# Kernel optimization log

Measured on AMD Instinct MI355X. Metric: run time of the kernel, lower is better.

Reference implementation:

```python
import jax, jax.numpy as jnp
import numpy as np

B = 8192
I = 1024
H = 1024


def setup_inputs() -> dict:
    key = jax.random.key(0)
    ks = jax.random.split(key, 7)
    s_in = 1.0 / np.sqrt(I)
    s_h = 1.0 / np.sqrt(H)
    return {
        "x_current": jax.random.normal(ks[0], (B, I), dtype=jnp.float32),
        "c_previous": jax.random.normal(ks[1], (B, H), dtype=jnp.float32),
        "h_previous": jax.random.normal(ks[2], (B, H), dtype=jnp.float32),
        # stacked gate weights, order (i, f, o, g); equivalent to 8 small nn.Linear
        "Wx": jax.random.normal(ks[3], (4 * H, I), dtype=jnp.float32) * s_in,
        "bx": jax.random.normal(ks[4], (4 * H,), dtype=jnp.float32) * s_in,
        "Wh": jax.random.normal(ks[5], (4 * H, H), dtype=jnp.float32) * s_h,
        "bh": jax.random.normal(ks[6], (4 * H,), dtype=jnp.float32) * s_h,
    }


def reference(x_current, c_previous, h_previous, Wx, bx, Wh, bh):
    # two fused GEMMs covering all 8 original linears: [B, 4H]
    gates = (jnp.einsum("bi,gi->bg", x_current, Wx) + bx
             + jnp.einsum("bh,gh->bg", h_previous, Wh) + bh)
    i_g, f_g, o_g, g_g = jnp.split(gates, 4, axis=-1)
    input_gate = jax.nn.sigmoid(i_g)
    forget_gate = jax.nn.sigmoid(f_g)
    output_gate = jax.nn.sigmoid(o_g)
    g_current = jnp.tanh(g_g)
    c_current = forget_gate * c_previous + input_gate * g_current
    h_current = output_gate * jnp.tanh(c_current)
    return (c_current, h_current)
```

## Files before the change

### kernel.cpp

```cpp
#include <hip/hip_runtime.h>
#include <hip/hip_bf16.h>

#define Bsz 8192
#define Isz 1024
#define Hsz 1024
#define Ksz 2048
#define Nsz 4096

#define BM 256
#define BN 256
#define BK 64
#define NT (Ksz / BK)

typedef __attribute__((ext_vector_type(8))) short bf16x8;
typedef __attribute__((ext_vector_type(4))) float f32x4;
typedef __attribute__((ext_vector_type(8))) unsigned short ushort8;

__device__ __forceinline__ void async_copy16(const void* g, void* l) {
  __builtin_amdgcn_global_load_lds(
      (const __attribute__((address_space(1))) void*)g,
      (__attribute__((address_space(3))) void*)l, 16, 0, 0);
}

__device__ __forceinline__ float fast_rcp(float x) {
  return __builtin_amdgcn_rcpf(x);
}
__device__ __forceinline__ float sigmoid_f(float x) {
  return fast_rcp(1.0f + __expf(-x));
}
__device__ __forceinline__ float tanh_f(float x) {
  x = fminf(15.0f, fmaxf(-15.0f, x));
  const float e = __expf(-2.0f * x);
  return (1.0f - e) * fast_rcp(1.0f + e);
}

__device__ __forceinline__ unsigned short bfc(float f) {
  return __builtin_bit_cast(unsigned short, __float2bfloat16(f));
}
__device__ __forceinline__ ushort8 cvt8v(float4 v0, float4 v1) {
  ushort8 o;
  o[0] = bfc(v0.x); o[1] = bfc(v0.y); o[2] = bfc(v0.z); o[3] = bfc(v0.w);
  o[4] = bfc(v1.x); o[5] = bfc(v1.y); o[6] = bfc(v1.z); o[7] = bfc(v1.w);
  return o;
}

__global__ __launch_bounds__(256) void prep_kernel(
    const float* __restrict__ x, const float* __restrict__ h,
    const float* __restrict__ Wx, const float* __restrict__ Wh,
    const float* __restrict__ bx, const float* __restrict__ bh,
    __hip_bfloat16* __restrict__ Abf, __hip_bfloat16* __restrict__ Wbf,
    float* __restrict__ bsum) {
  const int idx = blockIdx.x * 256 + threadIdx.x;
  const int ATH = (Bsz * Ksz) / 8;
  if (idx < ATH) {
    const int b = idx >> 8;
    const int k = (idx & 255) << 3;
    const float* src = (k < Isz) ? (x + (size_t)b * Isz + k)
                                 : (h + (size_t)b * Hsz + (k - Isz));
    const float4 v0 = ((const float4*)src)[0];
    const float4 v1 = ((const float4*)src)[1];
    *(ushort8*)(Abf + (size_t)b * Ksz + k) = cvt8v(v0, v1);
  } else {
    const int t2 = idx - ATH;
    const int r = t2 >> 8;
    const int k = (t2 & 255) << 3;
    const int hh = r >> 2, g = r & 3;
    const float* src = (k < Isz) ? (Wx + (size_t)(g * Hsz + hh) * Isz + k)
                                 : (Wh + (size_t)(g * Hsz + hh) * Hsz + (k - Isz));
    const float4 v0 = ((const float4*)src)[0];
    const float4 v1 = ((const float4*)src)[1];
    *(ushort8*)(Wbf + (size_t)r * Ksz + k) = cvt8v(v0, v1);
  }
  if (idx < Nsz) {
    const int hh = idx >> 2, g = idx & 3;
    bsum[idx] = bx[g * Hsz + hh] + bh[g * Hsz + hh];
  }
}

__global__ __launch_bounds__(512, 2) void lstm_gemm_kernel(
    const __hip_bfloat16* __restrict__ A,
    const __hip_bfloat16* __restrict__ W,
    const float* __restrict__ bsum,
    const float* __restrict__ c_prev,
    float* __restrict__ c_out,
    float* __restrict__ h_out) {
  __shared__ ulong2 smem_raw[8192];
  __hip_bfloat16* const As = (__hip_bfloat16*)smem_raw;
  __hip_bfloat16* const Bs = As + 2 * BM * BK;
  char* const smemc = (char*)smem_raw;

  const int tid = threadIdx.x;
  const int lane = tid & 63;
  const int wave = tid >> 6;
  const int wm = wave >> 2;
  const int wn = wave & 3;

  const int orig = blockIdx.x;
  const int swz = (orig & 7) * 64 + (orig >> 3);
  const int bx = swz & 31;
  const int by = swz >> 5;
  const int row0 = bx * BM;
  const int col0 = by * BN;

  const __hip_bfloat16* const Ag = A + (size_t)row0 * Ksz;
  const __hip_bfloat16* const Wg = W + (size_t)col0 * Ksz;

  const int sr = tid >> 3;
  const int so = ((tid & 7) ^ (sr & 7)) << 3;

  auto stage = [&](const __hip_bfloat16* gsrc, char* lhalf) {
#pragma unroll
    for (int p = 0; p < 2; ++p)
      async_copy16(gsrc + (size_t)(sr + p * 64) * Ksz,
                   lhalf + (tid + p * 512) * 16);
  };

  const int q = lane >> 4;
  const int cl = lane & 15;
  const int phi = cl & 7;
  const int swz0 = ((0 + q) ^ phi) << 3;
  const int swz1 = ((4 + q) ^ phi) << 3;
  const int aoff0 = (wm * 128 + cl) * BK + swz0;
  const int aoff1 = (wm * 128 + cl) * BK + swz1;
  const int boff0 = (wn * 64 + cl) * BK + swz0;
  const int boff1 = (wn * 64 + cl) * BK + swz1;

  stage(Ag + so, smemc);
  stage(Ag + (size_t)128 * Ksz + so, smemc + 16384);
  stage(Wg + so, smemc + 65536);
  stage(Wg + (size_t)128 * Ksz + so, smemc + 65536 + 16384);
  __builtin_amdgcn_sched_barrier(0);
  stage(Wg + BK + so, smemc + 65536 + 32768);
  stage(Wg + BK + (size_t)128 * Ksz + so, smemc + 65536 + 32768 + 16384);
  __builtin_amdgcn_sched_barrier(0);
  asm volatile("s_waitcnt vmcnt(4)" ::: "memory");
  __builtin_amdgcn_s_barrier();
  __builtin_amdgcn_sched_barrier(0);

  f32x4 acc[8][4] = {};

#define LDA(dst, m)                                                        \
  dst[0][0] = *(const bf16x8*)(Asb + aoff0 + (m) * (16 * BK));             \
  dst[0][1] = *(const bf16x8*)(Asb + aoff1 + (m) * (16 * BK));             \
  dst[1][0] = *(const bf16x8*)(Asb + aoff0 + ((m) + 1) * (16 * BK));       \
  dst[1][1] = *(const bf16x8*)(Asb + aoff1 + ((m) + 1) * (16 * BK));

#define CLUSTER(mi, p)                                                     \
  __builtin_amdgcn_s_setprio(1);                                           \
  _Pragma("unroll")                                                        \
  for (int n = 0; n < 4; ++n) {                                            \
    acc[mi][n] = __builtin_amdgcn_mfma_f32_16x16x32_bf16(                  \
        p[0][0], b0[n][0], acc[mi][n], 0, 0, 0);                           \
    acc[mi][n] = __builtin_amdgcn_mfma_f32_16x16x32_bf16(                  \
        p[0][1], b0[n][1], acc[mi][n], 0, 0, 0);                           \
    acc[(mi) + 1][n] = __builtin_amdgcn_mfma_f32_16x16x32_bf16(            \
        p[1][0], b0[n][0], acc[(mi) + 1][n], 0, 0, 0);                     \
    acc[(mi) + 1][n] = __builtin_amdgcn_mfma_f32_16x16x32_bf16(            \
        p[1][1], b0[n][1], acc[(mi) + 1][n], 0, 0, 0);                     \
  }                                                                        \
  __builtin_amdgcn_s_setprio(0);

  for (int t = 0; t < NT; ++t) {
    const __hip_bfloat16* const Asb = As + (t & 1) * (BM * BK);
    const __hip_bfloat16* const Bsb = Bs + (t & 1) * (BM * BK);
    char* const nA = smemc + (((t + 1) & 1) * 32768);
    char* const nB = smemc + 65536 + ((t & 1) * 32768);
    const int kA = (t + 1) * BK;
    const int kB = (t + 2) * BK;
    const bool doA = (t + 1) < NT;
    const bool doB = (t + 2) < NT;

    bf16x8 b0[4][2];
    bf16x8 aE[2][2], aO[2][2];

#pragma unroll
    for (int n = 0; n < 4; ++n) {
      b0[n][0] = *(const bf16x8*)(Bsb + boff0 + n * (16 * BK));
      b0[n][1] = *(const bf16x8*)(Bsb + boff1 + n * (16 * BK));
    }
    LDA(aE, 0)

    LDA(aO, 2)
    if (doA) stage(Ag + kA + so, nA);
    __builtin_amdgcn_sched_barrier(0);
    CLUSTER(0, aE)

    LDA(aE, 4)
    if (doA) stage(Ag + kA + (size_t)128 * Ksz + so, nA + 16384);
    __builtin_amdgcn_sched_barrier(0);
    CLUSTER(2, aO)

    __builtin_amdgcn_s_barrier();
    __builtin_amdgcn_sched_barrier(0);

    LDA(aO, 6)
    if (doB) stage(Wg + kB + so, nB);
    __builtin_amdgcn_sched_barrier(0);
    CLUSTER(4, aE)

    if (doB) stage(Wg + kB + (size_t)128 * Ksz + so, nB + 16384);
    __builtin_amdgcn_sched_barrier(0);
    CLUSTER(6, aO)

    if (t < NT - 2) {
      asm volatile("s_waitcnt vmcnt(4)" ::: "memory");
    } else if (t == NT - 2) {
      asm volatile("s_waitcnt vmcnt(0)" ::: "memory");
    }
    __builtin_amdgcn_s_barrier();
    __builtin_amdgcn_sched_barrier(0);
  }
#undef LDA
#undef CLUSTER

  __syncthreads();
  float* const E = (float*)smem_raw + wave * (16 * 68);

  float bj[4];
#pragma unroll
  for (int n = 0; n < 4; ++n)
    bj[n] = bsum[col0 + wn * 64 + n * 16 + cl];

  const int hw = (col0 >> 2) + wn * 16;
  const int r16 = lane >> 2;
  const int tt = lane & 3;

#pragma unroll
  for (int i = 0; i < 8; ++i) {
#pragma unroll
    for (int n = 0; n < 4; ++n)
#pragma unroll
      for (int r = 0; r < 4; ++r)
        E[(q * 4 + r) * 68 + n * 16 + cl] = acc[i][n][r] + bj[n];
    __builtin_amdgcn_wave_barrier();
    const float* Er = E + r16 * 68 + tt * 16;
    const float4 f0 = ((const float4*)Er)[0];
    const float4 f1 = ((const float4*)Er)[1];
    const float4 f2 = ((const float4*)Er)[2];
    const float4 f3 = ((const float4*)Er)[3];

    const int row = row0 + wm * 128 + i * 16 + r16;
    const size_t off = (size_t)row * Hsz + hw + tt * 4;
    const float4 cp4 = *(const float4*)(c_prev + off);
    float4 c4, h4;
    {
      const float cn = sigmoid_f(f0.y) * cp4.x + sigmoid_f(f0.x) * tanh_f(f0.w);
      c4.x = cn; h4.x = sigmoid_f(f0.z) * tanh_f(cn);
    }
    {
      const float cn = sigmoid_f(f1.y) * cp4.y + sigmoid_f(f1.x) * tanh_f(f1.w);
      c4.y = cn; h4.y = sigmoid_f(f1.z) * tanh_f(cn);
    }
    {
      const float cn = sigmoid_f(f2.y) * cp4.z + sigmoid_f(f2.x) * tanh_f(f2.w);
      c4.z = cn; h4.z = sigmoid_f(f2.z) * tanh_f(cn);
    }
    {
      const float cn = sigmoid_f(f3.y) * cp4.w + sigmoid_f(f3.x) * tanh_f(f3.w);
      c4.w = cn; h4.w = sigmoid_f(f3.z) * tanh_f(cn);
    }
    *(float4*)(c_out + off) = c4;
    *(float4*)(h_out + off) = h4;
    __builtin_amdgcn_wave_barrier();
  }
}

extern "C" void kernel_launch(void* const* d_in, const int* in_sizes, int n_in,
                              void* d_out, int out_size, void* d_ws,
                              size_t ws_size, hipStream_t stream) {
  (void)in_sizes; (void)n_in; (void)out_size; (void)ws_size;
  const float* x  = (const float*)d_in[0];
  const float* cp = (const float*)d_in[1];
  const float* hp = (const float*)d_in[2];
  const float* Wx = (const float*)d_in[3];
  const float* bx = (const float*)d_in[4];
  const float* Wh = (const float*)d_in[5];
  const float* bh = (const float*)d_in[6];

  __hip_bfloat16* Abf = (__hip_bfloat16*)d_ws;
  __hip_bfloat16* Wbf = Abf + (size_t)Bsz * Ksz;
  float* bsum = (float*)(Wbf + (size_t)Nsz * Ksz);

  float* c_out = (float*)d_out;
  float* h_out = c_out + (size_t)Bsz * Hsz;

  const int total_threads = (Bsz * Ksz) / 8 + (Nsz * Ksz) / 8;
  prep_kernel<<<total_threads / 256, 256, 0, stream>>>(x, hp, Wx, Wh, bx, bh,
                                                       Abf, Wbf, bsum);
  dim3 grid(Bsz / BM * (Nsz / BN));
  lstm_gemm_kernel<<<grid, 512, 0, stream>>>(Abf, Wbf, bsum, cp, c_out, h_out);
}
```

Before: 294.5 us.

## Triple-buffer W tiles and split MFMA clusters by K-half to drop mid-loop barrier

Shared memory grows so the W operand uses three rotating buffers instead of two. That removes the mid-iteration s_barrier that previously kept W prefetches from overwriting data still being read. The per-iteration MFMA schedule is also split into finer clusters, one per K-half, with LDS reads interleaved between them, and B fragments are loaded per K-half. The larger LDS footprint (160KB per block) may limit occupancy, given launch bounds of 2 blocks per CU.

After: 293.7 us. About the same (-0.3%).

```diff
diff --git a/kernel.cpp b/kernel.cpp
--- a/kernel.cpp
+++ b/kernel.cpp
@@ -11,6 +11,7 @@
 #define BN 256
 #define BK 64
 #define NT (Ksz / BK)
+#define BUF (BM * BK)
 
 typedef __attribute__((ext_vector_type(8))) short bf16x8;
 typedef __attribute__((ext_vector_type(4))) float f32x4;
@@ -84,10 +85,9 @@
     const float* __restrict__ c_prev,
     float* __restrict__ c_out,
     float* __restrict__ h_out) {
-  __shared__ ulong2 smem_raw[8192];
+  __shared__ ulong2 smem_raw[10240];
   __hip_bfloat16* const As = (__hip_bfloat16*)smem_raw;
-  __hip_bfloat16* const Bs = As + 2 * BM * BK;
-  char* const smemc = (char*)smem_raw;
+  __hip_bfloat16* const Bs = As + 2 * BUF;
 
   const int tid = threadIdx.x;
   const int lane = tid & 63;
@@ -125,13 +125,17 @@
   const int boff0 = (wn * 64 + cl) * BK + swz0;
   const int boff1 = (wn * 64 + cl) * BK + swz1;
 
-  stage(Ag + so, smemc);
-  stage(Ag + (size_t)128 * Ksz + so, smemc + 16384);
-  stage(Wg + so, smemc + 65536);
-  stage(Wg + (size_t)128 * Ksz + so, smemc + 65536 + 16384);
-  __builtin_amdgcn_sched_barrier(0);
-  stage(Wg + BK + so, smemc + 65536 + 32768);
-  stage(Wg + BK + (size_t)128 * Ksz + so, smemc + 65536 + 32768 + 16384);
+  const __hip_bfloat16* Bp0 = Bs;
+  const __hip_bfloat16* Bp1 = Bs + BUF;
+  const __hip_bfloat16* Bp2 = Bs + 2 * BUF;
+
+  stage(Ag + so, (char*)As);
+  stage(Ag + (size_t)128 * Ksz + so, (char*)As + 16384);
+  stage(Wg + so, (char*)Bs);
+  stage(Wg + (size_t)128 * Ksz + so, (char*)Bs + 16384);
+  __builtin_amdgcn_sched_barrier(0);
+  stage(Wg + BK + so, (char*)(Bs + BUF));
+  stage(Wg + BK + (size_t)128 * Ksz + so, (char*)(Bs + BUF) + 16384);
   __builtin_amdgcn_sched_barrier(0);
   asm volatile("s_waitcnt vmcnt(4)" ::: "memory");
   __builtin_amdgcn_s_barrier();
@@ -139,68 +143,66 @@
 
   f32x4 acc[8][4] = {};
 
-#define LDA(dst, m)                                                        \
-  dst[0][0] = *(const bf16x8*)(Asb + aoff0 + (m) * (16 * BK));             \
-  dst[0][1] = *(const bf16x8*)(Asb + aoff1 + (m) * (16 * BK));             \
-  dst[1][0] = *(const bf16x8*)(Asb + aoff0 + ((m) + 1) * (16 * BK));       \
-  dst[1][1] = *(const bf16x8*)(Asb + aoff1 + ((m) + 1) * (16 * BK));
-
-#define CLUSTER(mi, p)                                                     \
+#define SB0 __builtin_amdgcn_sched_barrier(0);
+
+#define LDA2(dst, m, ks)                                                   \
+  dst[0][ks] = *(const bf16x8*)(Asb + aoff##ks + (m) * (16 * BK));         \
+  dst[1][ks] = *(const bf16x8*)(Asb + aoff##ks + ((m) + 1) * (16 * BK));
+
+#define LDB(ks)                                                            \
+  _Pragma("unroll")                                                        \
+  for (int n = 0; n < 4; ++n)                                              \
+    b[n][ks] = *(const bf16x8*)(Bsb + boff##ks + n * (16 * BK));
+
+#define CL(mi, ks, p)                                                      \
   __builtin_amdgcn_s_setprio(1);                                           \
   _Pragma("unroll")                                                        \
   for (int n = 0; n < 4; ++n) {                                            \
     acc[mi][n] = __builtin_amdgcn_mfma_f32_16x16x32_bf16(                  \
-        p[0][0], b0[n][0], acc[mi][n], 0, 0, 0);                           \
-    acc[mi][n] = __builtin_amdgcn_mfma_f32_16x16x32_bf16(                  \
-        p[0][1], b0[n][1], acc[mi][n], 0, 0, 0);                           \
+        p[0][ks], b[n][ks], acc[mi][n], 0, 0, 0);                          \
     acc[(mi) + 1][n] = __builtin_amdgcn_mfma_f32_16x16x32_bf16(            \
-        p[1][0], b0[n][0], acc[(mi) + 1][n], 0, 0, 0);                     \
-    acc[(mi) + 1][n] = __builtin_amdgcn_mfma_f32_16x16x32_bf16(            \
-        p[1][1], b0[n][1], acc[(mi) + 1][n], 0, 0, 0);                     \
+        p[1][ks], b[n][ks], acc[(mi) + 1][n], 0, 0, 0);                    \
   }                                                                        \
-  __builtin_amdgcn_s_setprio(0);
+  __builtin_amdgcn_s_setprio(0);                                           \
+  __builtin_amdgcn_sched_barrier(0);
 
   for (int t = 0; t < NT; ++t) {
-    const __hip_bfloat16* const Asb = As + (t & 1) * (BM * BK);
-    const __hip_bfloat16* const Bsb = Bs + (t & 1) * (BM * BK);
-    char* const nA = smemc + (((t + 1) & 1) * 32768);
-    char* const nB = smemc + 65536 + ((t & 1) * 32768);
+    const __hip_bfloat16* const Asb = As + (t & 1) * BUF;
+    const __hip_bfloat16* const Bsb = Bp0;
+    char* const nA = (char*)As + ((t + 1) & 1) * 32768;
+    char* const nB = (char*)Bp2;
     const int kA = (t + 1) * BK;
     const int kB = (t + 2) * BK;
     const bool doA = (t + 1) < NT;
     const bool doB = (t + 2) < NT;
 
-    bf16x8 b0[4][2];
+    bf16x8 b[4][2];
     bf16x8 aE[2][2], aO[2][2];
 
-#pragma unroll
-    for (int n = 0; n < 4; ++n) {
-      b0[n][0] = *(const bf16x8*)(Bsb + boff0 + n * (16 * BK));
-      b0[n][1] = *(const bf16x8*)(Bsb + boff1 + n * (16 * BK));
-    }
-    LDA(aE, 0)
-
-    LDA(aO, 2)
+    LDB(0) LDA2(aE, 0, 0)
     if (doA) stage(Ag + kA + so, nA);
-    __builtin_amdgcn_sched_barrier(0);
-    CLUSTER(0, aE)
-
-    LDA(aE, 4)
+    SB0
+    CL(0, 0, aE)
+
+    LDB(1) LDA2(aE, 0, 1)
     if (doA) stage(Ag + kA + (size_t)128 * Ksz + so, nA + 16384);
-    __builtin_amdgcn_sched_barrier(0);
-    CLUSTER(2, aO)
-
-    __builtin_amdgcn_s_barrier();
-    __builtin_amdgcn_sched_barrier(0);
-
-    LDA(aO, 6)
+    SB0
+    CL(0, 1, aE)
+
+    LDA2(aO, 2, 0)
     if (doB) stage(Wg + kB + so, nB);
-    __builtin_amdgcn_sched_barrier(0);
-    CLUSTER(4, aE)
-
+    SB0
+    CL(2, 0, aO)
+
+    LDA2(aO, 2, 1)
     if (doB) stage(Wg + kB + (size_t)128 * Ksz + so, nB + 16384);
-    __builtin_amdgcn_sched_barrier(0);
-    CLUSTER(6, aO)
+    SB0
+    CL(2, 1, aO)
+
+    LDA2(aE, 4, 0) SB0 CL(4, 0, aE)
+    LDA2(aE, 4, 1) SB0 CL(4, 1, aE)
+    LDA2(aO, 6, 0) SB0 CL(6, 0, aO)
+    LDA2(aO, 6, 1) SB0 CL(6, 1, aO)
 
     if (t < NT - 2) {
       asm volatile("s_waitcnt vmcnt(4)" ::: "memory");
@@ -209,9 +211,14 @@
     }
     __builtin_amdgcn_s_barrier();
     __builtin_amdgcn_sched_barrier(0);
-  }
-#undef LDA
-#undef CLUSTER
+
+    const __hip_bfloat16* const tmp = Bp0;
+    Bp0 = Bp1; Bp1 = Bp2; Bp2 = tmp;
+  }
+#undef LDA2
+#undef LDB
+#undef CL
+#undef SB0
 
   __syncthreads();
   float* const E = (float*)smem_raw + wave * (16 * 68);
```
